# Kernel optimization log

Measured on AMD Instinct MI355X. Metric: run time of the kernel, lower is better.

## Reference

```python
import jax, jax.numpy as jnp
import numpy as np

H = 1024
R = 16


def setup_inputs() -> dict:
    key = jax.random.key(0)
    ks = jax.random.split(key, 9)
    s = 1.0 / np.sqrt(H)
    x = jax.random.normal(ks[0], (8192, H), dtype=jnp.float32)
    # gate (rule_attention): Linear(H, R)
    Wa = jax.random.uniform(ks[1], (H, R), minval=-s, maxval=s, dtype=jnp.float32)
    ba = jax.random.uniform(ks[2], (R,), minval=-s, maxval=s, dtype=jnp.float32)
    # stacked rule_heads: R x (Linear(H,H) -> ReLU -> Linear(H,H))
    W1 = jax.random.uniform(ks[3], (R, H, H), minval=-s, maxval=s, dtype=jnp.float32)
    b1 = jax.random.uniform(ks[4], (R, H), minval=-s, maxval=s, dtype=jnp.float32)
    W2 = jax.random.uniform(ks[5], (R, H, H), minval=-s, maxval=s, dtype=jnp.float32)
    b2 = jax.random.uniform(ks[6], (R, H), minval=-s, maxval=s, dtype=jnp.float32)
    # stacked rule_confidence: R x (Linear(H,1) -> Sigmoid)
    Wc = jax.random.uniform(ks[7], (R, H), minval=-s, maxval=s, dtype=jnp.float32)
    bc = jax.random.uniform(ks[8], (R,), minval=-s, maxval=s, dtype=jnp.float32)
    return {"x": x, "Wa": Wa, "ba": ba, "W1": W1, "b1": b1,
            "W2": W2, "b2": b2, "Wc": Wc, "bc": bc}


def reference(x, Wa, ba, W1, b1, W2, b2, Wc, bc):
    # gate: softmax over rules               [B, R]
    attention = jax.nn.softmax(x @ Wa + ba, axis=-1)
    # all rule MLPs as one batched matmul    [B, R, H]
    h = jax.nn.relu(jnp.einsum("bh,rhd->brd", x, W1) + b1)
    outputs = jnp.einsum("brd,rdo->bro", h, W2) + b2
    # per-rule confidence                    [B, R]
    confidences = jax.nn.sigmoid(jnp.einsum("bh,rh->br", x, Wc) + bc)
    # combine gate with confidence, renormalize, weighted sum over rules
    combined = attention * confidences
    combined = combined / (combined.sum(axis=-1, keepdims=True) + 1e-8)
    output = jnp.einsum("bro,br->bo", outputs, combined)  # [B, H]
    return output, confidences
```

## Files before the change

### kernel.cpp

```cpp
#include <hip/hip_runtime.h>

typedef __attribute__((ext_vector_type(8))) short short8;
typedef __attribute__((ext_vector_type(4))) float f32x4;

#define B_SZ 8192
#define H_SZ 1024
#define R_SZ 16

__device__ __forceinline__ unsigned short f2bf(float f) {
  union { float f; unsigned u; } v; v.f = f;
  unsigned u = v.u + 0x7FFFu + ((v.u >> 16) & 1u);
  return (unsigned short)(u >> 16);
}

__global__ __launch_bounds__(256) void tck_transpose(const float* __restrict__ src,
                                                     unsigned short* __restrict__ dst,
                                                     int rows, int cols) {
  __shared__ float t[32][33];
  size_t zoff = (size_t)blockIdx.z * (size_t)rows * cols;
  int c0 = blockIdx.x * 32, r0 = blockIdx.y * 32;
  int tx = threadIdx.x, ty = threadIdx.y;
#pragma unroll
  for (int i = 0; i < 4; ++i)
    t[ty + 8 * i][tx] = src[zoff + (size_t)(r0 + ty + 8 * i) * cols + c0 + tx];
  __syncthreads();
#pragma unroll
  for (int i = 0; i < 4; ++i)
    dst[zoff + (size_t)(c0 + ty + 8 * i) * rows + r0 + tx] = f2bf(t[tx][ty + 8 * i]);
}

__global__ __launch_bounds__(256) void twk_transpose_wa(const float* __restrict__ Wa,
                                                        float* __restrict__ WaT) {
  int t = blockIdx.x * 256 + threadIdx.x;
  int h = t >> 4, r = t & 15;
  WaT[r * H_SZ + h] = Wa[t];
}

__global__ __launch_bounds__(256) void gk_gate(const float* __restrict__ x,
                                               const float* __restrict__ WaT,
                                               const float* __restrict__ ba,
                                               const float* __restrict__ Wc,
                                               const float* __restrict__ bc,
                                               float* __restrict__ comb,
                                               float* __restrict__ conf,
                                               unsigned short* __restrict__ xb) {
  int b = blockIdx.x * 4 + (threadIdx.x >> 6);
  int l = threadIdx.x & 63;
  const float* xr = x + (size_t)b * H_SZ;
  unsigned short* xbr = xb + (size_t)b * H_SZ;
  float xv[16];
#pragma unroll
  for (int j = 0; j < 16; ++j) xv[j] = xr[l + 64 * j];
#pragma unroll
  for (int j = 0; j < 16; ++j) xbr[l + 64 * j] = f2bf(xv[j]);
  float la[16], lcf[16];
#pragma unroll
  for (int r = 0; r < 16; ++r) {
    float sa = 0.f, sc = 0.f;
#pragma unroll
    for (int j = 0; j < 16; ++j) {
      int h = l + 64 * j;
      sa += xv[j] * WaT[r * H_SZ + h];
      sc += xv[j] * Wc[r * H_SZ + h];
    }
#pragma unroll
    for (int off = 32; off > 0; off >>= 1) {
      sa += __shfl_xor(sa, off);
      sc += __shfl_xor(sc, off);
    }
    la[r] = sa + ba[r];
    lcf[r] = sc + bc[r];
  }
  float mx = la[0];
#pragma unroll
  for (int r = 1; r < 16; ++r) mx = fmaxf(mx, la[r]);
  float se = 0.f;
#pragma unroll
  for (int r = 0; r < 16; ++r) { la[r] = expf(la[r] - mx); se += la[r]; }
  float cb[16]; float cs = 0.f;
#pragma unroll
  for (int r = 0; r < 16; ++r) {
    float cf = 1.f / (1.f + expf(-lcf[r]));
    lcf[r] = cf;
    cb[r] = (la[r] / se) * cf;
    cs += cb[r];
  }
  float inv = 1.f / (cs + 1e-8f);
  if (l < 16) {
    float cv = 0.f, qv = 0.f;
#pragma unroll
    for (int r = 0; r < 16; ++r)
      if (r == l) { cv = lcf[r]; qv = cb[r] * inv; }
    conf[b * 16 + l] = cv;
    comb[b * 16 + l] = qv;
  }
}

__global__ __launch_bounds__(256) void redk_add(float* __restrict__ out,
                                                const float* __restrict__ p1) {
  size_t i = ((size_t)blockIdx.x * 256 + threadIdx.x) * 4;
  float4 a = *(const float4*)(out + i);
  float4 b = *(const float4*)(p1 + i);
  a.x += b.x; a.y += b.y; a.z += b.z; a.w += b.w;
  *(float4*)(out + i) = a;
}

__device__ __forceinline__ void gload16(const unsigned short* g, const unsigned short* l) {
  __builtin_amdgcn_global_load_lds(
      (const __attribute__((address_space(1))) unsigned int*)g,
      (__attribute__((address_space(3))) unsigned int*)(unsigned short*)l, 16, 0, 0);
}

#define RDA(DST, MH)                                                                   \
  _Pragma("unroll") for (int c = 0; c < 2; ++c)                                        \
  _Pragma("unroll") for (int f = 0; f < 4; ++f) {                                      \
    int ra = (MH) * 128 + wm * 64 + f * 16 + lc;                                       \
    DST[c][f] = *(const short8*)(bufp + ra * 64 + (((c * 4 + lr) ^ (ra & 7)) * 8));    \
  }
#define RDB(DST, NH)                                                                   \
  _Pragma("unroll") for (int c = 0; c < 2; ++c)                                        \
  _Pragma("unroll") for (int g = 0; g < 2; ++g) {                                      \
    int rb = (NH) * 128 + wn * 32 + g * 16 + lc;                                       \
    DST[c][g] = *(const short8*)(bufp + ABM + rb * 64 + (((c * 4 + lr) ^ (rb & 7)) * 8)); \
  }
#define MF(AS, BS, MH, NH)                                                             \
  __builtin_amdgcn_s_setprio(1);                                                       \
  _Pragma("unroll") for (int c = 0; c < 2; ++c)                                        \
  _Pragma("unroll") for (int f = 0; f < 4; ++f)                                        \
  _Pragma("unroll") for (int g = 0; g < 2; ++g)                                        \
    acc[(MH) * 4 + f][(NH) * 2 + g] = __builtin_amdgcn_mfma_f32_16x16x32_bf16(         \
        AS[c][f], BS[c][g], acc[(MH) * 4 + f][(NH) * 2 + g], 0, 0, 0);                 \
  __builtin_amdgcn_s_setprio(0);
#define LGKM0                                                                          \
  asm volatile("s_waitcnt lgkmcnt(0)" ::: "memory");                                   \
  __builtin_amdgcn_sched_barrier(0);

template <int MODE>
__global__ __launch_bounds__(512, 1) void g1k_gemm8(
    const unsigned short* __restrict__ A, int lda,
    const unsigned short* __restrict__ Bm, int ldb, int K,
    unsigned short* __restrict__ Hp, int ldh,
    const float* __restrict__ b1v,
    float* __restrict__ Out,
    const float* __restrict__ b2v,
    const float* __restrict__ comb,
    int r_base, int accum,
    float* __restrict__ Out2) {
  constexpr int ABM = 256 * 64;
  constexpr int BUFE = 2 * ABM;
  __shared__ unsigned short smem[2 * BUFE];

  const int tid = threadIdx.x;
  const int lane = tid & 63;
  const int wid = tid >> 6;
  const int wm = wid >> 2, wn = wid & 3;
  const int lr = lane >> 4, lc = lane & 15;
  const int bn0 = (MODE == 2 ? blockIdx.y : blockIdx.x) * 256;
  const int bm0 = (MODE == 2 ? blockIdx.x : blockIdx.y) * 256;
  const int KT = K >> 6;
  if (MODE == 2) {
    A += (size_t)blockIdx.z * (size_t)K;
    Bm += (size_t)blockIdx.z * (size_t)K;
  }

  f32x4 acc[8][4];
#pragma unroll
  for (int i = 0; i < 8; ++i)
#pragma unroll
    for (int j = 0; j < 4; ++j) acc[i][j] = {0.f, 0.f, 0.f, 0.f};

  auto stageA = [&](int buf, int kt, int h) {
#pragma unroll
    for (int q = 0; q < 2; ++q) {
      int idx = q * 512 + tid;
      int row = h * 128 + (idx >> 3);
      int ck = (idx & 7) ^ (row & 7);
      gload16(A + (size_t)(bm0 + row) * lda + kt * 64 + ck * 8,
              smem + buf * BUFE + h * 8192 + (q * 512 + (tid & ~63)) * 8);
    }
  };
  auto stageB = [&](int buf, int kt, int h) {
#pragma unroll
    for (int q = 0; q < 2; ++q) {
      int idx = q * 512 + tid;
      int row = h * 128 + (idx >> 3);
      int ck = (idx & 7) ^ (row & 7);
      gload16(Bm + (size_t)(bn0 + row) * ldb + kt * 64 + ck * 8,
              smem + buf * BUFE + ABM + h * 8192 + (q * 512 + (tid & ~63)) * 8);
    }
  };

  stageA(0, 0, 0); stageB(0, 0, 0); stageB(0, 0, 1); stageA(0, 0, 1);
  stageA(1, 1, 0); stageB(1, 1, 0); stageB(1, 1, 1);
  asm volatile("s_waitcnt vmcnt(6)" ::: "memory");
  __builtin_amdgcn_s_barrier();

  for (int t = 0; t < KT; ++t) {
    const unsigned short* bufp = smem + (t & 1) * BUFE;
    const int nb = (t & 1) ^ 1;
    const int cb = (t & 1);
    short8 a0[2][4], a1[2][4], b0[2][2], b1h[2][2];

    RDA(a0, 0)
    RDB(b0, 0)
    if (t + 1 < KT) stageA(nb, t + 1, 1);
    __builtin_amdgcn_s_barrier();
    LGKM0
    MF(a0, b0, 0, 0)
    __builtin_amdgcn_s_barrier();

    RDB(b1h, 1)
    if (t + 2 < KT) stageA(cb, t + 2, 0);
    __builtin_amdgcn_s_barrier();
    LGKM0
    MF(a0, b1h, 0, 1)
    __builtin_amdgcn_s_barrier();

    RDA(a1, 1)
    if (t + 2 < KT) stageB(cb, t + 2, 0);
    __builtin_amdgcn_s_barrier();
    LGKM0
    MF(a1, b1h, 1, 1)
    __builtin_amdgcn_s_barrier();

    if (t + 2 < KT) stageB(cb, t + 2, 1);
    __builtin_amdgcn_s_barrier();
    MF(a1, b0, 1, 0)
    asm volatile("s_waitcnt vmcnt(6)" ::: "memory");
    __builtin_amdgcn_s_barrier();
  }

#pragma unroll
  for (int i = 0; i < 8; ++i) {
#pragma unroll
    for (int j = 0; j < 4; ++j) {
      int m0 = bm0 + (i >> 2) * 128 + wm * 64 + (i & 3) * 16 + lr * 4;
      int n = bn0 + (j >> 1) * 128 + wn * 32 + (j & 1) * 16 + lc;
      f32x4 a = acc[i][j];
      if (MODE == 0) {
        int r = r_base + (n >> 10);
        int d = n & 1023;
        float bias = b1v[r * H_SZ + d];
#pragma unroll
        for (int jj = 0; jj < 4; ++jj) {
          float v = fmaxf(a[jj] + bias, 0.f) * comb[(size_t)(m0 + jj) * 16 + r];
          Hp[(size_t)(m0 + jj) * ldh + n] = f2bf(v);
        }
      } else {
        float* dst = blockIdx.z ? Out2 : Out;
#pragma unroll
        for (int jj = 0; jj < 4; ++jj) {
          size_t row = (size_t)(m0 + jj);
          float v = a[jj];
          if (accum) {
            v += dst[row * H_SZ + n];
          } else if (blockIdx.z == 0) {
            float bs = 0.f;
#pragma unroll
            for (int r = 0; r < 16; ++r)
              bs += comb[row * 16 + r] * b2v[r * H_SZ + n];
            v += bs;
          }
          dst[row * H_SZ + n] = v;
        }
      }
    }
  }
}
#undef RDA
#undef RDB
#undef MF
#undef LGKM0

__global__ __launch_bounds__(256) void g2s_gemm(
    const unsigned short* __restrict__ A, int lda,
    const unsigned short* __restrict__ B, int ldb,
    int K,
    float* __restrict__ Out,
    const float* __restrict__ b2v,
    const float* __restrict__ comb,
    int accum) {
  __shared__ short smem[16384];
  short* As = smem;
  short* Bs = smem + 8192;

  const int tid = threadIdx.x;
  const int lane = tid & 63;
  const int wid = tid >> 6;
  const int wm = wid >> 1, wn = wid & 1;
  const int lr = lane >> 4, lc = lane & 15;

  const int id = blockIdx.x;
  const int bm0 = (id & 63) * 128;
  const int bn0 = (id >> 6) * 128;

  int srow[4], ssc[4];
#pragma unroll
  for (int i = 0; i < 4; ++i) {
    int idx = i * 256 + tid;
    srow[i] = idx >> 3;
    ssc[i] = idx & 7;
  }

  const f32x4 zero = {0.f, 0.f, 0.f, 0.f};
  f32x4 acc[4][4];
#pragma unroll
  for (int i = 0; i < 4; ++i)
#pragma unroll
    for (int j = 0; j < 4; ++j) acc[i][j] = zero;

  const int KT = K >> 6;

  short8 va[4], vb[4];
#pragma unroll
  for (int i = 0; i < 4; ++i) {
    va[i] = *(const short8*)(A + (size_t)(bm0 + srow[i]) * lda + ssc[i] * 8);
    vb[i] = *(const short8*)(B + (size_t)(bn0 + srow[i]) * ldb + ssc[i] * 8);
  }

  for (int kt = 0; kt < KT; ++kt) {
    __syncthreads();
#pragma unroll
    for (int i = 0; i < 4; ++i) {
      *(short8*)(As + srow[i] * 64 + ((ssc[i] ^ (srow[i] & 7)) * 8)) = va[i];
      *(short8*)(Bs + srow[i] * 64 + ((ssc[i] ^ (srow[i] & 7)) * 8)) = vb[i];
    }
    __syncthreads();
    if (kt + 1 < KT) {
      int k0 = (kt + 1) << 6;
#pragma unroll
      for (int i = 0; i < 4; ++i) {
        va[i] = *(const short8*)(A + (size_t)(bm0 + srow[i]) * lda + k0 + ssc[i] * 8);
        vb[i] = *(const short8*)(B + (size_t)(bn0 + srow[i]) * ldb + k0 + ssc[i] * 8);
      }
    }
#pragma unroll
    for (int c = 0; c < 2; ++c) {
      short8 af[4], bfr[4];
#pragma unroll
      for (int f = 0; f < 4; ++f) {
        int ra = wm * 64 + f * 16 + lc;
        af[f] = *(const short8*)(As + ra * 64 + (((c * 4 + lr) ^ (ra & 7)) * 8));
        int rb = wn * 64 + f * 16 + lc;
        bfr[f] = *(const short8*)(Bs + rb * 64 + (((c * 4 + lr) ^ (rb & 7)) * 8));
      }
#pragma unroll
      for (int mf = 0; mf < 4; ++mf)
#pragma unroll
        for (int nf = 0; nf < 4; ++nf)
          acc[mf][nf] = __builtin_amdgcn_mfma_f32_16x16x32_bf16(af[mf], bfr[nf],
                                                                acc[mf][nf], 0, 0, 0);
    }
  }

#pragma unroll
  for (int mf = 0; mf < 4; ++mf) {
#pragma unroll
    for (int nf = 0; nf < 4; ++nf) {
      int m0 = bm0 + wm * 64 + mf * 16 + lr * 4;
      int n = bn0 + wn * 64 + nf * 16 + lc;
      f32x4 a = acc[mf][nf];
#pragma unroll
      for (int j = 0; j < 4; ++j) {
        size_t row = (size_t)(m0 + j);
        float v = a[j];
        if (accum) {
          v += Out[row * H_SZ + n];
        } else {
          float bs = 0.f;
#pragma unroll
          for (int r = 0; r < 16; ++r)
            bs += comb[row * 16 + r] * b2v[r * H_SZ + n];
          v += bs;
        }
        Out[row * H_SZ + n] = v;
      }
    }
  }
}

extern "C" void kernel_launch(void* const* d_in, const int* in_sizes, int n_in,
                              void* d_out, int out_size, void* d_ws, size_t ws_size,
                              hipStream_t stream) {
  if (n_in < 9) return;
  const float* x  = (const float*)d_in[0];
  const float* Wa = (const float*)d_in[1];
  const float* ba = (const float*)d_in[2];
  const float* W1 = (const float*)d_in[3];
  const float* b1 = (const float*)d_in[4];
  const float* W2 = (const float*)d_in[5];
  const float* b2 = (const float*)d_in[6];
  const float* Wc = (const float*)d_in[7];
  const float* bc = (const float*)d_in[8];

  float* out = (float*)d_out;
  float* conf = out + (size_t)B_SZ * H_SZ;

  char* w = (char*)d_ws;
  unsigned short* xb = (unsigned short*)w;  w += (size_t)B_SZ * H_SZ * 2;
  unsigned short* W1T = (unsigned short*)w; w += (size_t)R_SZ * H_SZ * H_SZ * 2;
  unsigned short* W2T = (unsigned short*)w; w += (size_t)R_SZ * H_SZ * H_SZ * 2;
  float* comb = (float*)w;                  w += (size_t)B_SZ * R_SZ * 4;
  float* WaT = (float*)w;                   w += (size_t)R_SZ * H_SZ * 4;
  unsigned short* Hp = (unsigned short*)w;
  size_t used = (size_t)(w - (char*)d_ws);

  int G = 16;
  while (G > 1 && used + (size_t)B_SZ * G * H_SZ * 2 > ws_size) G >>= 1;
  if (used + (size_t)B_SZ * G * H_SZ * 2 > ws_size) return;

  char* afterHp = (char*)Hp + (size_t)B_SZ * G * H_SZ * 2;
  float* part1 = (float*)afterHp;
  bool splitk = ((size_t)(afterHp - (char*)d_ws) + (size_t)B_SZ * H_SZ * 4 <= ws_size);

  dim3 tb(32, 8);
  tck_transpose<<<dim3(32, 32, 16), tb, 0, stream>>>(W1, W1T, H_SZ, H_SZ);
  tck_transpose<<<dim3(32, 512, 1), tb, 0, stream>>>(W2, W2T, R_SZ * H_SZ, H_SZ);
  twk_transpose_wa<<<dim3(64), dim3(256), 0, stream>>>(Wa, WaT);
  gk_gate<<<dim3(B_SZ / 4), dim3(256), 0, stream>>>(x, WaT, ba, Wc, bc, comb, conf, xb);

  int ngroups = R_SZ / G;
  for (int g = 0; g < ngroups; ++g) {
    g1k_gemm8<0><<<dim3(G * H_SZ / 256, B_SZ / 256), dim3(512), 0, stream>>>(
        xb, H_SZ,
        W1T + (size_t)g * G * H_SZ * H_SZ, H_SZ, H_SZ,
        Hp, G * H_SZ, b1, nullptr, nullptr, comb, g * G, 0, nullptr);
    if (splitk) {
      g1k_gemm8<2><<<dim3(B_SZ / 256, H_SZ / 256, 2), dim3(512), 0, stream>>>(
          Hp, G * H_SZ,
          W2T + (size_t)g * G * H_SZ, R_SZ * H_SZ, (G * H_SZ) / 2,
          nullptr, 0, nullptr, out, b2, comb, 0, (g > 0) ? 1 : 0, part1);
    } else {
      g2s_gemm<<<dim3(512), dim3(256), 0, stream>>>(
          Hp, G * H_SZ,
          W2T + (size_t)g * G * H_SZ, R_SZ * H_SZ, G * H_SZ,
          out, b2, comb, (g > 0) ? 1 : 0);
    }
  }
  if (splitk)
    redk_add<<<dim3((B_SZ * H_SZ) / (256 * 4)), dim3(256), 0, stream>>>(out, part1);
}
```

Measured before the change: 826.1 us.

## Store hidden activations and W2 in per-rule blocked layout and drop fallback GEMM

The hidden activation buffer Hp and the transposed W2 are now laid out as separate per-rule [rows x 1024] blocks instead of one wide row of G*1024. The second GEMM indexes rule blocks by k-tile, so each row stride is 1024 elements rather than 16K. The intent is to shorten strides and improve TLB and cache locality for both the Hp writes and the split-K reads. The non-split-K fallback kernel is removed, and split-K now always runs, with part1 space required when choosing G.

```diff
diff --git a/kernel.cpp b/kernel.cpp
--- a/kernel.cpp
+++ b/kernel.cpp
@@ -136,7 +136,7 @@
   __builtin_amdgcn_sched_barrier(0);
 
 template <int MODE>
-__global__ __launch_bounds__(512, 1) void g1k_gemm8(
+__global__ __launch_bounds__(512, 1) void g8r_gemm(
     const unsigned short* __restrict__ A, int lda,
     const unsigned short* __restrict__ Bm, int ldb, int K,
     unsigned short* __restrict__ Hp, int ldh,
@@ -148,6 +148,8 @@
     float* __restrict__ Out2) {
   constexpr int ABM = 256 * 64;
   constexpr int BUFE = 2 * ABM;
+  constexpr size_t ARULE = (size_t)B_SZ * H_SZ;
+  constexpr size_t BRULE = (size_t)H_SZ * H_SZ;
   __shared__ unsigned short smem[2 * BUFE];
 
   const int tid = threadIdx.x;
@@ -159,8 +161,8 @@
   const int bm0 = (MODE == 2 ? blockIdx.x : blockIdx.y) * 256;
   const int KT = K >> 6;
   if (MODE == 2) {
-    A += (size_t)blockIdx.z * (size_t)K;
-    Bm += (size_t)blockIdx.z * (size_t)K;
+    A += (size_t)blockIdx.z * (size_t)(K >> 10) * ARULE;
+    Bm += (size_t)blockIdx.z * (size_t)(K >> 10) * BRULE;
   }
 
   f32x4 acc[8][4];
@@ -175,8 +177,13 @@
       int idx = q * 512 + tid;
       int row = h * 128 + (idx >> 3);
       int ck = (idx & 7) ^ (row & 7);
-      gload16(A + (size_t)(bm0 + row) * lda + kt * 64 + ck * 8,
-              smem + buf * BUFE + h * 8192 + (q * 512 + (tid & ~63)) * 8);
+      const unsigned short* src;
+      if (MODE == 2)
+        src = A + (size_t)(kt >> 4) * ARULE + (size_t)(bm0 + row) * H_SZ +
+              (kt & 15) * 64 + ck * 8;
+      else
+        src = A + (size_t)(bm0 + row) * lda + kt * 64 + ck * 8;
+      gload16(src, smem + buf * BUFE + h * 8192 + (q * 512 + (tid & ~63)) * 8);
     }
   };
   auto stageB = [&](int buf, int kt, int h) {
@@ -185,8 +192,13 @@
       int idx = q * 512 + tid;
       int row = h * 128 + (idx >> 3);
       int ck = (idx & 7) ^ (row & 7);
-      gload16(Bm + (size_t)(bn0 + row) * ldb + kt * 64 + ck * 8,
-              smem + buf * BUFE + ABM + h * 8192 + (q * 512 + (tid & ~63)) * 8);
+      const unsigned short* src;
+      if (MODE == 2)
+        src = Bm + (size_t)(kt >> 4) * BRULE + (size_t)(bn0 + row) * H_SZ +
+              (kt & 15) * 64 + ck * 8;
+      else
+        src = Bm + (size_t)(bn0 + row) * ldb + kt * 64 + ck * 8;
+      gload16(src, smem + buf * BUFE + ABM + h * 8192 + (q * 512 + (tid & ~63)) * 8);
     }
   };
 
@@ -238,13 +250,14 @@
       int n = bn0 + (j >> 1) * 128 + wn * 32 + (j & 1) * 16 + lc;
       f32x4 a = acc[i][j];
       if (MODE == 0) {
-        int r = r_base + (n >> 10);
+        int rl = n >> 10;
+        int r = r_base + rl;
         int d = n & 1023;
         float bias = b1v[r * H_SZ + d];
 #pragma unroll
         for (int jj = 0; jj < 4; ++jj) {
           float v = fmaxf(a[jj] + bias, 0.f) * comb[(size_t)(m0 + jj) * 16 + r];
-          Hp[(size_t)(m0 + jj) * ldh + n] = f2bf(v);
+          Hp[(size_t)rl * ARULE + (size_t)(m0 + jj) * H_SZ + d] = f2bf(v);
         }
       } else {
         float* dst = blockIdx.z ? Out2 : Out;
@@ -271,113 +284,6 @@
 #undef RDB
 #undef MF
 #undef LGKM0
-
-__global__ __launch_bounds__(256) void g2s_gemm(
-    const unsigned short* __restrict__ A, int lda,
-    const unsigned short* __restrict__ B, int ldb,
-    int K,
-    float* __restrict__ Out,
-    const float* __restrict__ b2v,
-    const float* __restrict__ comb,
-    int accum) {
-  __shared__ short smem[16384];
-  short* As = smem;
-  short* Bs = smem + 8192;
-
-  const int tid = threadIdx.x;
-  const int lane = tid & 63;
-  const int wid = tid >> 6;
-  const int wm = wid >> 1, wn = wid & 1;
-  const int lr = lane >> 4, lc = lane & 15;
-
-  const int id = blockIdx.x;
-  const int bm0 = (id & 63) * 128;
-  const int bn0 = (id >> 6) * 128;
-
-  int srow[4], ssc[4];
-#pragma unroll
-  for (int i = 0; i < 4; ++i) {
-    int idx = i * 256 + tid;
-    srow[i] = idx >> 3;
-    ssc[i] = idx & 7;
-  }
-
-  const f32x4 zero = {0.f, 0.f, 0.f, 0.f};
-  f32x4 acc[4][4];
-#pragma unroll
-  for (int i = 0; i < 4; ++i)
-#pragma unroll
-    for (int j = 0; j < 4; ++j) acc[i][j] = zero;
-
-  const int KT = K >> 6;
-
-  short8 va[4], vb[4];
-#pragma unroll
-  for (int i = 0; i < 4; ++i) {
-    va[i] = *(const short8*)(A + (size_t)(bm0 + srow[i]) * lda + ssc[i] * 8);
-    vb[i] = *(const short8*)(B + (size_t)(bn0 + srow[i]) * ldb + ssc[i] * 8);
-  }
-
-  for (int kt = 0; kt < KT; ++kt) {
-    __syncthreads();
-#pragma unroll
-    for (int i = 0; i < 4; ++i) {
-      *(short8*)(As + srow[i] * 64 + ((ssc[i] ^ (srow[i] & 7)) * 8)) = va[i];
-      *(short8*)(Bs + srow[i] * 64 + ((ssc[i] ^ (srow[i] & 7)) * 8)) = vb[i];
-    }
-    __syncthreads();
-    if (kt + 1 < KT) {
-      int k0 = (kt + 1) << 6;
-#pragma unroll
-      for (int i = 0; i < 4; ++i) {
-        va[i] = *(const short8*)(A + (size_t)(bm0 + srow[i]) * lda + k0 + ssc[i] * 8);
-        vb[i] = *(const short8*)(B + (size_t)(bn0 + srow[i]) * ldb + k0 + ssc[i] * 8);
-      }
-    }
-#pragma unroll
-    for (int c = 0; c < 2; ++c) {
-      short8 af[4], bfr[4];
-#pragma unroll
-      for (int f = 0; f < 4; ++f) {
-        int ra = wm * 64 + f * 16 + lc;
-        af[f] = *(const short8*)(As + ra * 64 + (((c * 4 + lr) ^ (ra & 7)) * 8));
-        int rb = wn * 64 + f * 16 + lc;
-        bfr[f] = *(const short8*)(Bs + rb * 64 + (((c * 4 + lr) ^ (rb & 7)) * 8));
-      }
-#pragma unroll
-      for (int mf = 0; mf < 4; ++mf)
-#pragma unroll
-        for (int nf = 0; nf < 4; ++nf)
-          acc[mf][nf] = __builtin_amdgcn_mfma_f32_16x16x32_bf16(af[mf], bfr[nf],
-                                                                acc[mf][nf], 0, 0, 0);
-    }
-  }
-
-#pragma unroll
-  for (int mf = 0; mf < 4; ++mf) {
-#pragma unroll
-    for (int nf = 0; nf < 4; ++nf) {
-      int m0 = bm0 + wm * 64 + mf * 16 + lr * 4;
-      int n = bn0 + wn * 64 + nf * 16 + lc;
-      f32x4 a = acc[mf][nf];
-#pragma unroll
-      for (int j = 0; j < 4; ++j) {
-        size_t row = (size_t)(m0 + j);
-        float v = a[j];
-        if (accum) {
-          v += Out[row * H_SZ + n];
-        } else {
-          float bs = 0.f;
-#pragma unroll
-          for (int r = 0; r < 16; ++r)
-            bs += comb[row * 16 + r] * b2v[r * H_SZ + n];
-          v += bs;
-        }
-        Out[row * H_SZ + n] = v;
-      }
-    }
-  }
-}
 
 extern "C" void kernel_launch(void* const* d_in, const int* in_sizes, int n_in,
                               void* d_out, int out_size, void* d_ws, size_t ws_size,
@@ -406,37 +312,29 @@
   size_t used = (size_t)(w - (char*)d_ws);
 
   int G = 16;
-  while (G > 1 && used + (size_t)B_SZ * G * H_SZ * 2 > ws_size) G >>= 1;
-  if (used + (size_t)B_SZ * G * H_SZ * 2 > ws_size) return;
-
-  char* afterHp = (char*)Hp + (size_t)B_SZ * G * H_SZ * 2;
-  float* part1 = (float*)afterHp;
-  bool splitk = ((size_t)(afterHp - (char*)d_ws) + (size_t)B_SZ * H_SZ * 4 <= ws_size);
+  while (G > 1 &&
+         used + (size_t)B_SZ * G * H_SZ * 2 + (size_t)B_SZ * H_SZ * 4 > ws_size)
+    G >>= 1;
+  if (used + (size_t)B_SZ * G * H_SZ * 2 + (size_t)B_SZ * H_SZ * 4 > ws_size)
+    return;
+  float* part1 = (float*)((char*)Hp + (size_t)B_SZ * G * H_SZ * 2);
 
   dim3 tb(32, 8);
   tck_transpose<<<dim3(32, 32, 16), tb, 0, stream>>>(W1, W1T, H_SZ, H_SZ);
-  tck_transpose<<<dim3(32, 512, 1), tb, 0, stream>>>(W2, W2T, R_SZ * H_SZ, H_SZ);
+  tck_transpose<<<dim3(32, 32, 16), tb, 0, stream>>>(W2, W2T, H_SZ, H_SZ);
   twk_transpose_wa<<<dim3(64), dim3(256), 0, stream>>>(Wa, WaT);
   gk_gate<<<dim3(B_SZ / 4), dim3(256), 0, stream>>>(x, WaT, ba, Wc, bc, comb, conf, xb);
 
   int ngroups = R_SZ / G;
   for (int g = 0; g < ngroups; ++g) {
-    g1k_gemm8<0><<<dim3(G * H_SZ / 256, B_SZ / 256), dim3(512), 0, stream>>>(
+    g8r_gemm<0><<<dim3(G * H_SZ / 256, B_SZ / 256), dim3(512), 0, stream>>>(
         xb, H_SZ,
         W1T + (size_t)g * G * H_SZ * H_SZ, H_SZ, H_SZ,
-        Hp, G * H_SZ, b1, nullptr, nullptr, comb, g * G, 0, nullptr);
-    if (splitk) {
-      g1k_gemm8<2><<<dim3(B_SZ / 256, H_SZ / 256, 2), dim3(512), 0, stream>>>(
-          Hp, G * H_SZ,
-          W2T + (size_t)g * G * H_SZ, R_SZ * H_SZ, (G * H_SZ) / 2,
-          nullptr, 0, nullptr, out, b2, comb, 0, (g > 0) ? 1 : 0, part1);
-    } else {
-      g2s_gemm<<<dim3(512), dim3(256), 0, stream>>>(
-          Hp, G * H_SZ,
-          W2T + (size_t)g * G * H_SZ, R_SZ * H_SZ, G * H_SZ,
-          out, b2, comb, (g > 0) ? 1 : 0);
-    }
-  }
-  if (splitk)
-    redk_add<<<dim3((B_SZ * H_SZ) / (256 * 4)), dim3(256), 0, stream>>>(out, part1);
-}
+        Hp, 0, b1, nullptr, nullptr, comb, g * G, 0, nullptr);
+    g8r_gemm<2><<<dim3(B_SZ / 256, H_SZ / 256, 2), dim3(512), 0, stream>>>(
+        Hp, 0,
+        W2T + (size_t)g * G * H_SZ * H_SZ, 0, (G * H_SZ) / 2,
+        nullptr, 0, nullptr, out, b2, comb, 0, (g > 0) ? 1 : 0, part1);
+  }
+  redk_add<<<dim3((B_SZ * H_SZ) / (256 * 4)), dim3(256), 0, stream>>>(out, part1);
+}
```

Result: no change. 842.1 us (+1.9%).
